# Performance work log

Measured on AMD Instinct MI355X. Metric: run time of the kernel, lower is better.

## Reference

```python
import jax, jax.numpy as jnp
import numpy as np

B, S = 16, 4096
E_ENC, E_DEC, H = 1024, 1024, 512


def setup_inputs() -> dict:
    key = jax.random.key(0)
    ks = jax.random.split(key, 8)
    sc_e = 1.0 / np.sqrt(E_ENC)
    sc_d = 1.0 / np.sqrt(E_DEC)
    sc_h = 1.0 / np.sqrt(H)
    return {
        "encoder_hiddens": jax.random.normal(ks[0], (B, S, E_ENC), jnp.float32),
        "decoder_hidden": jax.random.normal(ks[1], (B, E_DEC), jnp.float32),
        "We": jax.random.uniform(ks[2], (E_ENC, H), jnp.float32, -sc_e, sc_e),
        "be": jax.random.uniform(ks[3], (H,), jnp.float32, -sc_e, sc_e),
        "Wd": jax.random.uniform(ks[4], (E_DEC, H), jnp.float32, -sc_d, sc_d),
        "bd": jax.random.uniform(ks[5], (H,), jnp.float32, -sc_d, sc_d),
        "Wo": jax.random.uniform(ks[6], (H, 1), jnp.float32, -sc_h, sc_h),
        "bo": jax.random.uniform(ks[7], (1,), jnp.float32, -sc_h, sc_h),
    }


def reference(encoder_hiddens, decoder_hidden, We, be, Wd, bd, Wo, bo):
    # Additive (Bahdanau) attention.
    # enc_proj: [B,S,H]; dec_proj: [B,1,H] broadcast over sequence.
    enc_proj = jnp.einsum("bse,eh->bsh", encoder_hiddens, We) + be
    dec_proj = jnp.einsum("bd,dh->bh", decoder_hidden, Wd) + bd
    e = jnp.tanh(enc_proj + dec_proj[:, None, :])          # [B,S,H]
    scores = jnp.einsum("bsh,h->bs", e, Wo[:, 0]) + bo[0]  # [B,S]
    attn = jax.nn.softmax(scores, axis=-1)                 # [B,S]
    context = jnp.einsum("bs,bse->be", attn, encoder_hiddens)  # [B,E_ENC]
    return context
```

## Files before the change

kernel.cpp:

```cpp
#include <hip/hip_runtime.h>
#include <hip/hip_bf16.h>
#include <math.h>

#define B_ 16
#define S_ 4096
#define E_ 1024
#define H_ 512

#define BM 128
#define BN 128
#define BK 64
#define NCHUNK (E_ / BK)

typedef short bf16x8 __attribute__((ext_vector_type(8)));
typedef unsigned short u16x8 __attribute__((ext_vector_type(8)));
typedef float f32x4 __attribute__((ext_vector_type(4)));

__device__ inline unsigned short f2bf(float x) {
    __hip_bfloat16 h = __float2bfloat16(x);
    return *(unsigned short*)&h;
}
__device__ inline float bf2f(unsigned short u) {
    unsigned int x = ((unsigned int)u) << 16;
    float f;
    __builtin_memcpy(&f, &x, 4);
    return f;
}
__device__ __forceinline__ void gld16(const unsigned short* g, unsigned short* l) {
    __builtin_amdgcn_global_load_lds(
        (const __attribute__((address_space(1))) void*)g,
        (__attribute__((address_space(3))) void*)l, 16, 0, 0);
}

__global__ __launch_bounds__(256) void prep_conv_kernel(
    const float* __restrict__ enc, const float* __restrict__ We,
    const float* __restrict__ dec, const float* __restrict__ Wd,
    const float* __restrict__ bd, const float* __restrict__ be,
    unsigned short* __restrict__ WeTcB, float* __restrict__ dp,
    unsigned short* __restrict__ encB) {
    __shared__ float red[4][64];
    int bid = blockIdx.x, t = threadIdx.x;
    if (bid < 64) {
        int c = bid >> 2, n0t = (bid & 3) * 128;
#pragma unroll 4
        for (int it = 0; it < 32; ++it) {
            int o = it * 256 + t;
            int n_rel = o >> 6, within = o & 63;
            int cp = within >> 3, j = within & 7;
            int n = n0t + n_rel;
            int k = c * 64 + ((cp ^ (n & 7)) << 3) + j;
            WeTcB[c * 32768 + n * 64 + within] = f2bf(We[(size_t)k * H_ + n]);
        }
    } else if (bid < 192) {
        int id = bid - 64;
        int b = id >> 3, hc = id & 7;
        int h = hc * 64 + (t & 63);
        int ec = t >> 6;
        const float* dr = dec + b * E_ + ec * 256;
        const float* wp = Wd + (size_t)(ec * 256) * H_ + h;
        float acc = 0.f;
#pragma unroll 8
        for (int e = 0; e < 256; ++e) acc = fmaf(dr[e], wp[(size_t)e * H_], acc);
        red[ec][t & 63] = acc;
        __syncthreads();
        if (t < 64) {
            int hh = hc * 64 + t;
            dp[b * H_ + hh] = red[0][t] + red[1][t] + red[2][t] + red[3][t] + bd[hh] + be[hh];
        }
    } else {
        size_t base = ((size_t)(bid - 192) * 256 + t) * 16;
        const float* ep = enc + base;
        unsigned short* op = encB + base;
        float4 v0 = *(const float4*)(ep);
        float4 v1 = *(const float4*)(ep + 4);
        float4 v2 = *(const float4*)(ep + 8);
        float4 v3 = *(const float4*)(ep + 12);
        u16x8 u0, u1;
        u0[0] = f2bf(v0.x); u0[1] = f2bf(v0.y); u0[2] = f2bf(v0.z); u0[3] = f2bf(v0.w);
        u0[4] = f2bf(v1.x); u0[5] = f2bf(v1.y); u0[6] = f2bf(v1.z); u0[7] = f2bf(v1.w);
        u1[0] = f2bf(v2.x); u1[1] = f2bf(v2.y); u1[2] = f2bf(v2.z); u1[3] = f2bf(v2.w);
        u1[4] = f2bf(v3.x); u1[5] = f2bf(v3.y); u1[6] = f2bf(v3.z); u1[7] = f2bf(v3.w);
        *(u16x8*)(op) = u0;
        *(u16x8*)(op + 8) = u1;
    }
}

__global__ __launch_bounds__(256, 3) void scores_gemm_kernel(
    const unsigned short* __restrict__ encB, const unsigned short* __restrict__ WeTcB,
    const float* __restrict__ Wo, const float* __restrict__ dp,
    float* __restrict__ parts) {
    __shared__ unsigned short sA[BM * BK];
    __shared__ unsigned short sB[BN * BK];
    __shared__ float sRed[2][BM];

    int tid = threadIdx.x;
    int w = tid >> 6, l = tid & 63;
    int l16 = l & 15, quad = l >> 4;
    int wm = w & 1, wn = w >> 1;
    int nt = blockIdx.x & 3;
    size_t mt = blockIdx.x >> 2;
    size_t m0 = mt * BM;
    int n0 = nt * BN;
    int b = (int)(m0 >> 12);

    int lrow = l >> 3, lcp = l & 7;
    int qa = lcp ^ (lrow & 7);
    const unsigned short* gA = encB + (m0 + w * 8 + lrow) * E_ + qa * 8;
    const unsigned short* gB = WeTcB + (size_t)n0 * BK + (w * 8) * BK + l * 8;
    unsigned short* sAb = sA + (w * 8) * BK;
    unsigned short* sBb = sB + (w * 8) * BK;

    f32x4 acc[4][4];
#pragma unroll
    for (int i = 0; i < 4; ++i)
#pragma unroll
        for (int j = 0; j < 4; ++j) acc[i][j] = (f32x4)0.f;

    int arow = (wm * 64 + l16) * BK;
    int brow = (wn * 64 + l16) * BK;
    int sw = l16 & 7;

    for (int c = 0; c < NCHUNK; ++c) {
        __syncthreads();
        int k0 = c * BK;
#pragma unroll
        for (int i = 0; i < 4; ++i) {
            gld16(gA + (size_t)i * 32 * E_ + k0, sAb + i * 32 * BK);
            gld16(gB + (size_t)c * (H_ * BK) + i * 32 * BK, sBb + i * 32 * BK);
        }
        __syncthreads();
#pragma unroll
        for (int half = 0; half < 2; ++half) {
            int koff = (((half * 4 + quad) ^ sw) << 3);
            bf16x8 aR[4], bR[4];
#pragma unroll
            for (int i = 0; i < 4; ++i)
                aR[i] = *(const bf16x8*)(sA + arow + i * 16 * BK + koff);
#pragma unroll
            for (int j = 0; j < 4; ++j)
                bR[j] = *(const bf16x8*)(sB + brow + j * 16 * BK + koff);
#pragma unroll
            for (int i = 0; i < 4; ++i)
#pragma unroll
                for (int j = 0; j < 4; ++j)
                    acc[i][j] = __builtin_amdgcn_mfma_f32_16x16x32_bf16(aR[i], bR[j], acc[i][j], 0, 0, 0);
        }
    }

    float dpv[4], wov[4];
    const float* dpb = dp + b * H_;
#pragma unroll
    for (int j = 0; j < 4; ++j) {
        int h = n0 + wn * 64 + j * 16 + l16;
        dpv[j] = dpb[h];
        wov[j] = Wo[h];
    }
#pragma unroll
    for (int i = 0; i < 4; ++i)
#pragma unroll
        for (int r = 0; r < 4; ++r) {
            float s = 0.f;
#pragma unroll
            for (int j = 0; j < 4; ++j) {
                float x = acc[i][j][r] + dpv[j];
                float e = __expf(2.f * x);
                s += (1.f - 2.f / (e + 1.f)) * wov[j];
            }
            s += __shfl_xor(s, 1, 64);
            s += __shfl_xor(s, 2, 64);
            s += __shfl_xor(s, 4, 64);
            s += __shfl_xor(s, 8, 64);
            if (l16 == 0) sRed[wn][wm * 64 + i * 16 + quad * 4 + r] = s;
        }
    __syncthreads();
    if (tid < BM) {
        int s_in = (int)(m0 & (S_ - 1)) + tid;
        parts[(size_t)(nt * B_ + b) * S_ + s_in] = sRed[0][tid] + sRed[1][tid];
    }
}

__global__ __launch_bounds__(256) void softmax_kernel(float* __restrict__ parts) {
    int b = blockIdx.x, tid = threadIdx.x;
    const float4* p0 = (const float4*)(parts + (size_t)(0 * B_ + b) * S_);
    const float4* p1 = (const float4*)(parts + (size_t)(1 * B_ + b) * S_);
    const float4* p2 = (const float4*)(parts + (size_t)(2 * B_ + b) * S_);
    const float4* p3 = (const float4*)(parts + (size_t)(3 * B_ + b) * S_);
    float4* row = (float4*)(parts + (size_t)b * S_);
    float4 v[4];
    float m = -1e30f;
#pragma unroll
    for (int i = 0; i < 4; ++i) {
        int idx = i * 256 + tid;
        float4 a0 = p0[idx], a1 = p1[idx], a2 = p2[idx], a3 = p3[idx];
        v[i].x = a0.x + a1.x + a2.x + a3.x;
        v[i].y = a0.y + a1.y + a2.y + a3.y;
        v[i].z = a0.z + a1.z + a2.z + a3.z;
        v[i].w = a0.w + a1.w + a2.w + a3.w;
        m = fmaxf(m, fmaxf(fmaxf(v[i].x, v[i].y), fmaxf(v[i].z, v[i].w)));
    }
    for (int off = 32; off; off >>= 1) m = fmaxf(m, __shfl_xor(m, off, 64));
    __shared__ float redm[4];
    __shared__ float reds[4];
    if ((tid & 63) == 0) redm[tid >> 6] = m;
    __syncthreads();
    m = fmaxf(fmaxf(redm[0], redm[1]), fmaxf(redm[2], redm[3]));
    float s = 0.f;
#pragma unroll
    for (int i = 0; i < 4; ++i) {
        v[i].x = __expf(v[i].x - m); v[i].y = __expf(v[i].y - m);
        v[i].z = __expf(v[i].z - m); v[i].w = __expf(v[i].w - m);
        s += (v[i].x + v[i].y) + (v[i].z + v[i].w);
    }
    for (int off = 32; off; off >>= 1) s += __shfl_xor(s, off, 64);
    if ((tid & 63) == 0) reds[tid >> 6] = s;
    __syncthreads();
    s = reds[0] + reds[1] + reds[2] + reds[3];
    float inv = 1.f / s;
#pragma unroll
    for (int i = 0; i < 4; ++i) {
        int idx = i * 256 + tid;
        row[idx] = make_float4(v[i].x * inv, v[i].y * inv, v[i].z * inv, v[i].w * inv);
    }
}

__global__ __launch_bounds__(256) void ctx_partial_bf16(
    const unsigned short* __restrict__ encB, const float* __restrict__ attn,
    float* __restrict__ part) {
    int b = blockIdx.x >> 5;
    int c = blockIdx.x & 31;
    int s0 = c * 128;
    int tid = threadIdx.x;
    __shared__ float w[128];
    if (tid < 128) w[tid] = attn[(size_t)b * S_ + s0 + tid];
    __syncthreads();
    int e8 = (tid & 127) * 8;
    int sh = tid >> 7;
    const unsigned short* base = encB + ((size_t)b * S_ + s0 + sh * 64) * E_ + e8;
    const float* wp = w + sh * 64;
    float acc[8];
#pragma unroll
    for (int t = 0; t < 8; ++t) acc[t] = 0.f;
    for (int s = 0; s < 64; s += 8) {
        u16x8 v[8];
#pragma unroll
        for (int u = 0; u < 8; ++u) v[u] = *(const u16x8*)(base + (size_t)(s + u) * E_);
#pragma unroll
        for (int u = 0; u < 8; ++u) {
            float ws = wp[s + u];
#pragma unroll
            for (int t = 0; t < 8; ++t) acc[t] = fmaf(ws, bf2f(v[u][t]), acc[t]);
        }
    }
    float* po = part + ((size_t)(b * 64 + c * 2 + sh)) * E_ + e8;
    *(float4*)(po) = make_float4(acc[0], acc[1], acc[2], acc[3]);
    *(float4*)(po + 4) = make_float4(acc[4], acc[5], acc[6], acc[7]);
}

__global__ __launch_bounds__(256) void ctx_reduce(const float* __restrict__ part,
                                                  float* __restrict__ out, int nch) {
    int idx = blockIdx.x * 256 + threadIdx.x;
    int b = idx >> 10;
    int e = idx & 1023;
    const float* p = part + (size_t)b * nch * E_ + e;
    float s0 = 0.f, s1 = 0.f, s2 = 0.f, s3 = 0.f;
    for (int c = 0; c < nch; c += 4) {
        s0 += p[(size_t)(c + 0) * E_];
        s1 += p[(size_t)(c + 1) * E_];
        s2 += p[(size_t)(c + 2) * E_];
        s3 += p[(size_t)(c + 3) * E_];
    }
    out[idx] = (s0 + s1) + (s2 + s3);
}

extern "C" void kernel_launch(void* const* d_in, const int* in_sizes, int n_in,
                              void* d_out, int out_size, void* d_ws, size_t ws_size,
                              hipStream_t stream) {
    const float* enc = (const float*)d_in[0];
    const float* dec = (const float*)d_in[1];
    const float* We  = (const float*)d_in[2];
    const float* be  = (const float*)d_in[3];
    const float* Wd  = (const float*)d_in[4];
    const float* bd  = (const float*)d_in[5];
    const float* Wo  = (const float*)d_in[6];
    float* out = (float*)d_out;

    char* wsp = (char*)d_ws;
    unsigned short* WeTcB = (unsigned short*)wsp;
    float* dp = (float*)(wsp + (1 << 20));
    float* parts = (float*)(wsp + (1 << 20) + (64 << 10));
    float* part = (float*)(wsp + (4 << 20));
    unsigned short* encB = (unsigned short*)(wsp + (8 << 20));
    float* attn = parts;

    prep_conv_kernel<<<192 + 16384, 256, 0, stream>>>(enc, We, dec, Wd, bd, be,
                                                      WeTcB, dp, encB);
    scores_gemm_kernel<<<(B_ * S_ / BM) * (H_ / BN), 256, 0, stream>>>(
        encB, WeTcB, Wo, dp, parts);
    softmax_kernel<<<B_, 256, 0, stream>>>(parts);
    ctx_partial_bf16<<<B_ * 32, 256, 0, stream>>>(encB, attn, part);
    ctx_reduce<<<B_ * E_ / 256, 256, 0, stream>>>(part, out, 64);
}
```

Baseline: 495.9 us.

## Remap GEMM blocks per XCD and defer softmax normalization into context kernels

```diff
diff --git a/kernel.cpp b/kernel.cpp
--- a/kernel.cpp
+++ b/kernel.cpp
@@ -97,8 +97,11 @@
     int w = tid >> 6, l = tid & 63;
     int l16 = l & 15, quad = l >> 4;
     int wm = w & 1, wn = w >> 1;
-    int nt = blockIdx.x & 3;
-    size_t mt = blockIdx.x >> 2;
+    int bid = blockIdx.x;
+    int xcd = bid & 7;
+    int sq = bid >> 3;
+    int nt = sq & 3;
+    size_t mt = (size_t)((sq >> 2) << 3) + xcd;
     size_t m0 = mt * BM;
     int n0 = nt * BN;
     int b = (int)(m0 >> 12);
@@ -179,13 +182,13 @@
     }
 }
 
-__global__ __launch_bounds__(256) void softmax_kernel(float* __restrict__ parts) {
+__global__ __launch_bounds__(256) void stats_kernel(const float* __restrict__ parts,
+                                                    float2* __restrict__ stats) {
     int b = blockIdx.x, tid = threadIdx.x;
     const float4* p0 = (const float4*)(parts + (size_t)(0 * B_ + b) * S_);
     const float4* p1 = (const float4*)(parts + (size_t)(1 * B_ + b) * S_);
     const float4* p2 = (const float4*)(parts + (size_t)(2 * B_ + b) * S_);
     const float4* p3 = (const float4*)(parts + (size_t)(3 * B_ + b) * S_);
-    float4* row = (float4*)(parts + (size_t)b * S_);
     float4 v[4];
     float m = -1e30f;
 #pragma unroll
@@ -207,31 +210,31 @@
     float s = 0.f;
 #pragma unroll
     for (int i = 0; i < 4; ++i) {
-        v[i].x = __expf(v[i].x - m); v[i].y = __expf(v[i].y - m);
-        v[i].z = __expf(v[i].z - m); v[i].w = __expf(v[i].w - m);
-        s += (v[i].x + v[i].y) + (v[i].z + v[i].w);
+        s += __expf(v[i].x - m) + __expf(v[i].y - m);
+        s += __expf(v[i].z - m) + __expf(v[i].w - m);
     }
     for (int off = 32; off; off >>= 1) s += __shfl_xor(s, off, 64);
     if ((tid & 63) == 0) reds[tid >> 6] = s;
     __syncthreads();
-    s = reds[0] + reds[1] + reds[2] + reds[3];
-    float inv = 1.f / s;
-#pragma unroll
-    for (int i = 0; i < 4; ++i) {
-        int idx = i * 256 + tid;
-        row[idx] = make_float4(v[i].x * inv, v[i].y * inv, v[i].z * inv, v[i].w * inv);
+    if (tid == 0) {
+        stats[b] = make_float2(m, reds[0] + reds[1] + reds[2] + reds[3]);
     }
 }
 
 __global__ __launch_bounds__(256) void ctx_partial_bf16(
-    const unsigned short* __restrict__ encB, const float* __restrict__ attn,
-    float* __restrict__ part) {
+    const unsigned short* __restrict__ encB, const float* __restrict__ parts,
+    const float2* __restrict__ stats, float* __restrict__ part) {
     int b = blockIdx.x >> 5;
     int c = blockIdx.x & 31;
     int s0 = c * 128;
     int tid = threadIdx.x;
     __shared__ float w[128];
-    if (tid < 128) w[tid] = attn[(size_t)b * S_ + s0 + tid];
+    if (tid < 128) {
+        size_t idx = (size_t)b * S_ + s0 + tid;
+        float x = parts[(size_t)(0 * B_) * S_ + idx] + parts[(size_t)(1 * B_) * S_ + idx] +
+                  parts[(size_t)(2 * B_) * S_ + idx] + parts[(size_t)(3 * B_) * S_ + idx];
+        w[tid] = __expf(x - stats[b].x);
+    }
     __syncthreads();
     int e8 = (tid & 127) * 8;
     int sh = tid >> 7;
@@ -257,19 +260,20 @@
 }
 
 __global__ __launch_bounds__(256) void ctx_reduce(const float* __restrict__ part,
-                                                  float* __restrict__ out, int nch) {
+                                                  const float2* __restrict__ stats,
+                                                  float* __restrict__ out) {
     int idx = blockIdx.x * 256 + threadIdx.x;
     int b = idx >> 10;
     int e = idx & 1023;
-    const float* p = part + (size_t)b * nch * E_ + e;
+    const float* p = part + (size_t)b * 64 * E_ + e;
     float s0 = 0.f, s1 = 0.f, s2 = 0.f, s3 = 0.f;
-    for (int c = 0; c < nch; c += 4) {
+    for (int c = 0; c < 64; c += 4) {
         s0 += p[(size_t)(c + 0) * E_];
         s1 += p[(size_t)(c + 1) * E_];
         s2 += p[(size_t)(c + 2) * E_];
         s3 += p[(size_t)(c + 3) * E_];
     }
-    out[idx] = (s0 + s1) + (s2 + s3);
+    out[idx] = ((s0 + s1) + (s2 + s3)) * (1.f / stats[b].y);
 }
 
 extern "C" void kernel_launch(void* const* d_in, const int* in_sizes, int n_in,
@@ -287,16 +291,16 @@
     char* wsp = (char*)d_ws;
     unsigned short* WeTcB = (unsigned short*)wsp;
     float* dp = (float*)(wsp + (1 << 20));
+    float2* stats = (float2*)(wsp + (1 << 20) + (32 << 10));
     float* parts = (float*)(wsp + (1 << 20) + (64 << 10));
     float* part = (float*)(wsp + (4 << 20));
     unsigned short* encB = (unsigned short*)(wsp + (8 << 20));
-    float* attn = parts;
 
     prep_conv_kernel<<<192 + 16384, 256, 0, stream>>>(enc, We, dec, Wd, bd, be,
                                                       WeTcB, dp, encB);
     scores_gemm_kernel<<<(B_ * S_ / BM) * (H_ / BN), 256, 0, stream>>>(
         encB, WeTcB, Wo, dp, parts);
-    softmax_kernel<<<B_, 256, 0, stream>>>(parts);
-    ctx_partial_bf16<<<B_ * 32, 256, 0, stream>>>(encB, attn, part);
-    ctx_reduce<<<B_ * E_ / 256, 256, 0, stream>>>(part, out, 64);
-}
+    stats_kernel<<<B_, 256, 0, stream>>>(parts, stats);
+    ctx_partial_bf16<<<B_ * 32, 256, 0, stream>>>(encB, parts, stats, part);
+    ctx_reduce<<<B_ * E_ / 256, 256, 0, stream>>>(part, stats, out);
+}
```

Result: faster. 485.3 us (-2.1%).
